# Kernel tuning notes

Measured on AMD Instinct MI355X. Metric: run time of the kernel, lower is better.

Reference implementation:

```python
import jax, jax.numpy as jnp
import numpy as np

B, C, H, W, D = 8, 192, 128, 128, 64


def setup_inputs() -> dict:
    key = jax.random.key(0)
    ks = jax.random.split(key, 9)
    s = 0.1
    return {
        'x': jax.random.normal(ks[0], (B, C, H, W), jnp.float32),
        'Wi': jax.random.normal(ks[1], (D, C), jnp.float32) * s,   # proj_in weight
        'bi': jax.random.normal(ks[2], (D,), jnp.float32) * s,
        'W_ih': jax.random.normal(ks[3], (3 * D, D), jnp.float32) * s,  # GRUCell weight_ih (r,z,n)
        'W_hh': jax.random.normal(ks[4], (3 * D, D), jnp.float32) * s,  # GRUCell weight_hh
        'b_ih': jax.random.normal(ks[5], (3 * D,), jnp.float32) * s,
        'b_hh': jax.random.normal(ks[6], (3 * D,), jnp.float32) * s,
        'Wo': jax.random.normal(ks[7], (C, D), jnp.float32) * s,   # proj_out weight
        'bo': jax.random.normal(ks[8], (C,), jnp.float32) * s,
    }


def _gru_scan(seq, W_ih, W_hh, b_ih, b_hh):
    # seq: (N, T, D). PyTorch GRUCell gate order: r, z, n.
    N, T, Dh = seq.shape[0], seq.shape[1], W_hh.shape[1]
    x_gates = jnp.einsum('ntd,gd->ntg', seq, W_ih) + b_ih  # (N, T, 3D), precomputed
    h0 = jnp.zeros((N, Dh), seq.dtype)

    def step(h, xg):
        hg = h @ W_hh.T + b_hh
        xr, xz, xn = jnp.split(xg, 3, axis=-1)
        hr, hz, hn = jnp.split(hg, 3, axis=-1)
        r = jax.nn.sigmoid(xr + hr)
        z = jax.nn.sigmoid(xz + hz)
        n = jnp.tanh(xn + r * hn)
        h_new = (1.0 - z) * n + z * h
        return h_new, h_new

    _, hs = jax.lax.scan(step, h0, jnp.swapaxes(x_gates, 0, 1))  # (T, N, D)
    return jnp.swapaxes(hs, 0, 1)  # (N, T, D)


def _scan_direction(x, Wi, bi, W_ih, W_hh, b_ih, b_hh, Wo, bo, transpose, reverse):
    b, c, h, w = x.shape
    # arrange to (B, A, T, C): scan along T (W for row scans, H for column scans)
    xs = jnp.transpose(x, (0, 3, 2, 1)) if transpose else jnp.transpose(x, (0, 2, 3, 1))
    if reverse:
        xs = xs[:, :, ::-1, :]
    A, T = xs.shape[1], xs.shape[2]
    seq = xs.reshape(b * A, T, c) @ Wi.T + bi              # proj_in -> (N, T, D)
    hs = _gru_scan(seq, W_ih, W_hh, b_ih, b_hh)            # (N, T, D)
    out = hs @ Wo.T + bo                                   # proj_out -> (N, T, C)
    out = out.reshape(b, A, T, c)
    if reverse:
        out = out[:, :, ::-1, :]
    return jnp.transpose(out, (0, 3, 2, 1)) if transpose else jnp.transpose(out, (0, 3, 1, 2))


def reference(x, Wi, bi, W_ih, W_hh, b_ih, b_hh, Wo, bo):
    p = (Wi, bi, W_ih, W_hh, b_ih, b_hh, Wo, bo)
    right = _scan_direction(x, *p, transpose=False, reverse=False)
    down = _scan_direction(x, *p, transpose=True, reverse=False)
    left = _scan_direction(x, *p, transpose=False, reverse=True)
    up = _scan_direction(x, *p, transpose=True, reverse=True)
    return (right + down + left + up) / 4.0
```

## Files before the change

kernel.cpp:

```cpp
#include <hip/hip_runtime.h>

#define Cn   192
#define Dn   64
#define G3   192
#define HWn  16384
#define NSp  131072L
#define Tn   128

typedef unsigned short u16;
typedef __attribute__((ext_vector_type(8))) short s8v;
typedef __attribute__((ext_vector_type(4))) float f4v;

__device__ __forceinline__ float bf2f(u16 u){
  union { unsigned int i; float f; } v; v.i = ((unsigned int)u) << 16; return v.f;
}
__device__ __forceinline__ u16 f2bf(float f){
  union { float f; unsigned int u; } v; v.f = f;
  return (u16)((v.u + 0x7FFFu + ((v.u >> 16) & 1u)) >> 16);
}
__device__ __forceinline__ s8v load8_f32_as_bf16(const float* __restrict__ p){
  s8v r;
  #pragma unroll
  for (int i = 0; i < 8; i++) r[i] = (short)f2bf(p[i]);
  return r;
}
__device__ __forceinline__ float ex2f(float x){
#if __has_builtin(__builtin_amdgcn_exp2f)
  return __builtin_amdgcn_exp2f(x);
#else
  float r; asm("v_exp_f32 %0, %1" : "=v"(r) : "v"(x)); return r;
#endif
}
__device__ __forceinline__ float rcpa(float x){
#if __has_builtin(__builtin_amdgcn_rcpf)
  return __builtin_amdgcn_rcpf(x);
#else
  float r; asm("v_rcp_f32 %0, %1" : "=v"(r) : "v"(x)); return r;
#endif
}

#define SC_RZ (-1.4426950408889634f)
#define SC_N  (-2.8853900817779268f)

__global__ __launch_bounds__(256) void k_wcomb(const float* __restrict__ Wi, const float* __restrict__ bi,
                                               const float* __restrict__ W_ih, const float* __restrict__ b_ih,
                                               u16* __restrict__ wcomb, float* __restrict__ bcomb){
  if (blockIdx.x < 144) {
    int idx = blockIdx.x * 256 + threadIdx.x;
    int g = idx / 192, c = idx - g * 192;
    float acc = 0.f;
    #pragma unroll 8
    for (int d = 0; d < 64; d++)
      acc += W_ih[g * 64 + d] * Wi[d * 192 + c];
    float sc = (g >= 128) ? SC_N : SC_RZ;
    wcomb[g * 192 + c] = f2bf(sc * acc);
  } else if (threadIdx.x < 192) {
    int g = threadIdx.x;
    float acc = b_ih[g];
    for (int d = 0; d < 64; d++)
      acc += W_ih[g * 64 + d] * bi[d];
    float sc = (g >= 128) ? SC_N : SC_RZ;
    bcomb[g] = sc * acc;
  }
}

__global__ __launch_bounds__(256) void k_gates(const float* __restrict__ x, const u16* __restrict__ wcomb,
                                               const float* __restrict__ bcomb, u16* __restrict__ G){
  __shared__ u16 xT[64][200];
  const int tid = threadIdx.x;
  const int wave = tid >> 6, lane = tid & 63;
  const int col = lane & 15, kq = lane >> 4;
  const long s0 = (long)blockIdx.x * 64;
  const int b   = (int)(s0 >> 14);
  const int hw0 = (int)(s0 & 16383);

  s8v bfrag[3][6];
  #pragma unroll
  for (int j = 0; j < 3; j++) {
    int g = wave * 48 + j * 16 + col;
    #pragma unroll
    for (int kc = 0; kc < 6; kc++)
      bfrag[j][kc] = *(const s8v*)(wcomb + g * 192 + kc * 32 + kq * 8);
  }

  for (int idx = tid; idx < 192 * 16; idx += 256) {
    int c  = idx >> 4;
    int s4 = (idx & 15) * 4;
    float4 v = *(const float4*)(x + (long)(b * 192 + c) * HWn + hw0 + s4);
    xT[s4 + 0][c] = f2bf(v.x); xT[s4 + 1][c] = f2bf(v.y);
    xT[s4 + 2][c] = f2bf(v.z); xT[s4 + 3][c] = f2bf(v.w);
  }
  __syncthreads();

  f4v acc[4][3];
  #pragma unroll
  for (int m = 0; m < 4; m++)
    #pragma unroll
    for (int j = 0; j < 3; j++) acc[m][j] = (f4v){0.f, 0.f, 0.f, 0.f};

  #pragma unroll
  for (int kc = 0; kc < 6; kc++) {
    #pragma unroll
    for (int m = 0; m < 4; m++) {
      s8v a = *(const s8v*)(&xT[m * 16 + col][kc * 32 + kq * 8]);
      #pragma unroll
      for (int j = 0; j < 3; j++)
        acc[m][j] = __builtin_amdgcn_mfma_f32_16x16x32_bf16(a, bfrag[j][kc], acc[m][j], 0, 0, 0);
    }
  }

  #pragma unroll
  for (int j = 0; j < 3; j++) {
    int g = wave * 48 + j * 16 + col;
    float bias = bcomb[g];
    #pragma unroll
    for (int m = 0; m < 4; m++) {
      #pragma unroll
      for (int r = 0; r < 4; r++) {
        long srow = s0 + m * 16 + kq * 4 + r;
        G[srow * 192 + g] = f2bf(acc[m][j][r] + bias);
      }
    }
  }
}

__global__ __launch_bounds__(256) void k_scan(const u16* __restrict__ G, const float* __restrict__ W_hh,
                                              const float* __restrict__ b_hh, u16* __restrict__ Hall){
  __shared__ u16 ha[2][16][72];
  const int tid = threadIdx.x;
  const int w = tid >> 6, lane = tid & 63;
  const int col = lane & 15, kq = lane >> 4;
  const int dir  = blockIdx.x >> 6;
  const int sblk = blockIdx.x & 63;
  const int doff = 16 * w + 4 * kq;

  s8v afrag[3][2];
  f4v biasf[3];
  #pragma unroll
  for (int g3 = 0; g3 < 3; g3++) {
    float sc = (g3 == 2) ? SC_N : SC_RZ;
    const float* wr = W_hh + (g3 * 64 + 16 * w + col) * 64;
    #pragma unroll
    for (int kc = 0; kc < 2; kc++) {
      s8v f;
      #pragma unroll
      for (int i = 0; i < 4; i++) f[i]     = (short)f2bf(sc * wr[kc * 32 +      4 * kq + i]);
      #pragma unroll
      for (int i = 0; i < 4; i++) f[4 + i] = (short)f2bf(sc * wr[kc * 32 + 16 + 4 * kq + i]);
      afrag[g3][kc] = f;
    }
    const float* bb = b_hh + g3 * 64 + doff;
    biasf[g3] = (f4v){ sc * bb[0], sc * bb[1], sc * bb[2], sc * bb[3] };
  }

  const int seq = sblk * 16 + col;
  const int b = seq >> 7, a = seq & 127;
  long base; int stride;
  if ((dir & 1) == 0) { base = ((long)(b * 128 + a)) * 128; stride = 1;   }
  else                { base = (long)b * 16384 + a;         stride = 128; }
  const int rev = dir >> 1;
  u16* __restrict__ Hs = Hall + (long)dir * (NSp * 64);

  for (int i = tid; i < 2 * 16 * 72; i += 256) ((u16*)ha)[i] = 0;
  float hold[4] = {0.f, 0.f, 0.f, 0.f};

  uint2 xr, xz, xn;
  {
    int tp = rev ? 127 : 0;
    const u16* gp = G + (base + (long)tp * stride) * 192 + doff;
    xr = *(const uint2*)(gp);
    xz = *(const uint2*)(gp + 64);
    xn = *(const uint2*)(gp + 128);
  }
  __syncthreads();

  int p = 0;
  for (int t = 0; t < 128; t++) {
    uint2 nxr, nxz, nxn;
    if (t < 127) {
      int tp2 = rev ? (126 - t) : (t + 1);
      const u16* gp2 = G + (base + (long)tp2 * stride) * 192 + doff;
      nxr = *(const uint2*)(gp2);
      nxz = *(const uint2*)(gp2 + 64);
      nxn = *(const uint2*)(gp2 + 128);
    }

    union BU { ushort4 q[2]; s8v v; } u0, u1;
    u0.q[0] = *(const ushort4*)(&ha[p][col][ 0 + 4 * kq]);
    u0.q[1] = *(const ushort4*)(&ha[p][col][16 + 4 * kq]);
    u1.q[0] = *(const ushort4*)(&ha[p][col][32 + 4 * kq]);
    u1.q[1] = *(const ushort4*)(&ha[p][col][48 + 4 * kq]);

    f4v acc0 = biasf[0], acc1 = biasf[1], acc2 = biasf[2];
    acc0 = __builtin_amdgcn_mfma_f32_16x16x32_bf16(afrag[0][0], u0.v, acc0, 0, 0, 0);
    acc1 = __builtin_amdgcn_mfma_f32_16x16x32_bf16(afrag[1][0], u0.v, acc1, 0, 0, 0);
    acc2 = __builtin_amdgcn_mfma_f32_16x16x32_bf16(afrag[2][0], u0.v, acc2, 0, 0, 0);
    acc0 = __builtin_amdgcn_mfma_f32_16x16x32_bf16(afrag[0][1], u1.v, acc0, 0, 0, 0);
    acc1 = __builtin_amdgcn_mfma_f32_16x16x32_bf16(afrag[1][1], u1.v, acc1, 0, 0, 0);
    acc2 = __builtin_amdgcn_mfma_f32_16x16x32_bf16(afrag[2][1], u1.v, acc2, 0, 0, 0);

    u16* px = (u16*)&xr; u16* pz = (u16*)&xz; u16* pn = (u16*)&xn;
    ushort4 hv; u16* hvp = (u16*)&hv;
    #pragma unroll
    for (int r = 0; r < 4; r++) {
      float rr = rcpa(1.f + ex2f(bf2f(px[r]) + acc0[r]));
      float zz = rcpa(1.f + ex2f(bf2f(pz[r]) + acc1[r]));
      float nn = 2.f * rcpa(1.f + ex2f(bf2f(pn[r]) + rr * acc2[r])) - 1.f;
      float h  = nn + zz * (hold[r] - nn);
      hold[r] = h;
      hvp[r] = f2bf(h);
    }

    *(ushort4*)(&ha[p ^ 1][col][doff]) = hv;
    long posc = base + (long)(rev ? (127 - t) : t) * stride;
    *(ushort4*)(Hs + posc * 64 + doff) = hv;
    if (t < 127) { xr = nxr; xz = nxz; xn = nxn; }
    __syncthreads();
    p ^= 1;
  }
}

__global__ __launch_bounds__(256) void k_out(const u16* __restrict__ Hall, const float* __restrict__ Wo,
                                             const float* __restrict__ bo, float* __restrict__ out){
  __shared__ u16 hs4[64][72];
  const int tid = threadIdx.x;
  const int wave = tid >> 6, lane = tid & 63;
  const int col = lane & 15, kq = lane >> 4;
  const long s0 = (long)blockIdx.x * 64;
  const int b   = (int)(s0 >> 14);
  const int hw0 = (int)(s0 & 16383);

  s8v bfrag[3][2]; f4v biasf[3];
  #pragma unroll
  for (int j = 0; j < 3; j++) {
    int g = wave * 48 + j * 16 + col;
    bfrag[j][0] = load8_f32_as_bf16(Wo + g * 64 + kq * 8);
    bfrag[j][1] = load8_f32_as_bf16(Wo + g * 64 + 32 + kq * 8);
    float bb = bo[g];
    biasf[j] = (f4v){bb, bb, bb, bb};
  }

  for (int idx = tid; idx < 64 * 16; idx += 256) {
    int sl = idx >> 4;
    int d4 = (idx & 15) * 4;
    long p = (s0 + sl) * 64 + d4;
    float a0 = 0.f, a1 = 0.f, a2 = 0.f, a3 = 0.f;
    #pragma unroll
    for (int dd = 0; dd < 4; dd++) {
      uint2 v = *(const uint2*)(Hall + dd * (NSp * 64) + p);
      u16* pv = (u16*)&v;
      a0 += bf2f(pv[0]); a1 += bf2f(pv[1]); a2 += bf2f(pv[2]); a3 += bf2f(pv[3]);
    }
    ushort4 o;
    o.x = f2bf(0.25f * a0); o.y = f2bf(0.25f * a1);
    o.z = f2bf(0.25f * a2); o.w = f2bf(0.25f * a3);
    *(ushort4*)(&hs4[sl][d4]) = o;
  }
  __syncthreads();

  f4v acc[4][3];
  #pragma unroll
  for (int m = 0; m < 4; m++)
    #pragma unroll
    for (int j = 0; j < 3; j++) acc[m][j] = biasf[j];

  #pragma unroll
  for (int kc = 0; kc < 2; kc++) {
    #pragma unroll
    for (int m = 0; m < 4; m++) {
      s8v a = *(const s8v*)(&hs4[m * 16 + col][kc * 32 + kq * 8]);
      #pragma unroll
      for (int j = 0; j < 3; j++)
        acc[m][j] = __builtin_amdgcn_mfma_f32_16x16x32_bf16(a, bfrag[j][kc], acc[m][j], 0, 0, 0);
    }
  }

  #pragma unroll
  for (int j = 0; j < 3; j++) {
    int g = wave * 48 + j * 16 + col;
    #pragma unroll
    for (int m = 0; m < 4; m++) {
      float4 v;
      v.x = acc[m][j][0]; v.y = acc[m][j][1];
      v.z = acc[m][j][2]; v.w = acc[m][j][3];
      long addr = ((long)(b * 192 + g) << 14) + hw0 + m * 16 + kq * 4;
      *(float4*)(out + addr) = v;
    }
  }
}

extern "C" void kernel_launch(void* const* d_in, const int* in_sizes, int n_in,
                              void* d_out, int out_size, void* d_ws, size_t ws_size,
                              hipStream_t stream){
  const float* x    = (const float*)d_in[0];
  const float* Wi   = (const float*)d_in[1];
  const float* bi   = (const float*)d_in[2];
  const float* W_ih = (const float*)d_in[3];
  const float* W_hh = (const float*)d_in[4];
  const float* b_ih = (const float*)d_in[5];
  const float* b_hh = (const float*)d_in[6];
  const float* Wo   = (const float*)d_in[7];
  const float* bo   = (const float*)d_in[8];

  char* ws = (char*)d_ws;
  u16*   wcomb = (u16*)(ws);
  float* bcomb = (float*)(ws + 73728);
  u16*   G     = (u16*)(ws + 74496);
  u16*   Hall  = (u16*)(ws + 50406144);

  k_wcomb<<<145,  256, 0, stream>>>(Wi, bi, W_ih, b_ih, wcomb, bcomb);
  k_gates<<<2048, 256, 0, stream>>>(x, wcomb, bcomb, G);
  k_scan <<<256,  256, 0, stream>>>(G, W_hh, b_hh, Hall);
  k_out  <<<2048, 256, 0, stream>>>(Hall, Wo, bo, (float*)d_out);
}
```

Baseline: 332.3 us.

## Run GRU scan in one wave with hidden state kept in MFMA registers

The recurrent scan kernel now uses a single 64-thread wave per block of 16 sequences instead of four waves. Each step's new hidden state is packed to bf16 and fed directly as the MFMA B operand from registers. This drops the shared-memory round trip and the per-step __syncthreads barrier. The r/z hidden biases are folded into the precomputed gate bias. In exchange, each wave issues four times as many MFMAs and gate evaluations per step, which lengthens per-step work on each CU and raises register pressure.

New measurement: 376.5 us. 1.13x slower.

```diff
diff --git a/kernel.cpp b/kernel.cpp
--- a/kernel.cpp
+++ b/kernel.cpp
@@ -44,6 +44,7 @@
 
 __global__ __launch_bounds__(256) void k_wcomb(const float* __restrict__ Wi, const float* __restrict__ bi,
                                                const float* __restrict__ W_ih, const float* __restrict__ b_ih,
+                                               const float* __restrict__ b_hh,
                                                u16* __restrict__ wcomb, float* __restrict__ bcomb){
   if (blockIdx.x < 144) {
     int idx = blockIdx.x * 256 + threadIdx.x;
@@ -59,6 +60,7 @@
     float acc = b_ih[g];
     for (int d = 0; d < 64; d++)
       acc += W_ih[g * 64 + d] * bi[d];
+    if (g < 128) acc += b_hh[g];
     float sc = (g >= 128) ? SC_N : SC_RZ;
     bcomb[g] = sc * acc;
   }
@@ -124,22 +126,18 @@
   }
 }
 
-__global__ __launch_bounds__(256) void k_scan(const u16* __restrict__ G, const float* __restrict__ W_hh,
-                                              const float* __restrict__ b_hh, u16* __restrict__ Hall){
-  __shared__ u16 ha[2][16][72];
-  const int tid = threadIdx.x;
-  const int w = tid >> 6, lane = tid & 63;
+__global__ __launch_bounds__(64, 1) void k_scan(const u16* __restrict__ G, const float* __restrict__ W_hh,
+                                                const float* __restrict__ b_hh, u16* __restrict__ Hall){
+  const int lane = threadIdx.x & 63;
   const int col = lane & 15, kq = lane >> 4;
   const int dir  = blockIdx.x >> 6;
   const int sblk = blockIdx.x & 63;
-  const int doff = 16 * w + 4 * kq;
-
-  s8v afrag[3][2];
-  f4v biasf[3];
-  #pragma unroll
-  for (int g3 = 0; g3 < 3; g3++) {
-    float sc = (g3 == 2) ? SC_N : SC_RZ;
-    const float* wr = W_hh + (g3 * 64 + 16 * w + col) * 64;
+
+  s8v afrag[12][2];
+  #pragma unroll
+  for (int j = 0; j < 12; j++) {
+    float sc = (j >= 8) ? SC_N : SC_RZ;
+    const float* wr = W_hh + (j * 16 + col) * 64;
     #pragma unroll
     for (int kc = 0; kc < 2; kc++) {
       s8v f;
@@ -147,10 +145,14 @@
       for (int i = 0; i < 4; i++) f[i]     = (short)f2bf(sc * wr[kc * 32 +      4 * kq + i]);
       #pragma unroll
       for (int i = 0; i < 4; i++) f[4 + i] = (short)f2bf(sc * wr[kc * 32 + 16 + 4 * kq + i]);
-      afrag[g3][kc] = f;
-    }
-    const float* bb = b_hh + g3 * 64 + doff;
-    biasf[g3] = (f4v){ sc * bb[0], sc * bb[1], sc * bb[2], sc * bb[3] };
+      afrag[j][kc] = f;
+    }
+  }
+  f4v biasn[4];
+  #pragma unroll
+  for (int jp = 0; jp < 4; jp++) {
+    const float* bb = b_hh + 128 + jp * 16 + 4 * kq;
+    biasn[jp] = (f4v){SC_N * bb[0], SC_N * bb[1], SC_N * bb[2], SC_N * bb[3]};
   }
 
   const int seq = sblk * 16 + col;
@@ -159,64 +161,83 @@
   if ((dir & 1) == 0) { base = ((long)(b * 128 + a)) * 128; stride = 1;   }
   else                { base = (long)b * 16384 + a;         stride = 128; }
   const int rev = dir >> 1;
+  const long pd = rev ? -(long)stride : (long)stride;
   u16* __restrict__ Hs = Hall + (long)dir * (NSp * 64);
 
-  for (int i = tid; i < 2 * 16 * 72; i += 256) ((u16*)ha)[i] = 0;
-  float hold[4] = {0.f, 0.f, 0.f, 0.f};
-
-  uint2 xr, xz, xn;
-  {
-    int tp = rev ? 127 : 0;
-    const u16* gp = G + (base + (long)tp * stride) * 192 + doff;
-    xr = *(const uint2*)(gp);
-    xz = *(const uint2*)(gp + 64);
-    xn = *(const uint2*)(gp + 128);
-  }
-  __syncthreads();
-
-  int p = 0;
+  const long pos0 = base + (long)(rev ? 127 : 0) * stride;
+  const u16* gq = G  + pos0 * 192 + 4 * kq;
+  u16*       hq = Hs + pos0 * 64  + 4 * kq;
+
+  uint2 xc[12];
+  #pragma unroll
+  for (int g3 = 0; g3 < 3; g3++)
+    #pragma unroll
+    for (int jp = 0; jp < 4; jp++)
+      xc[g3 * 4 + jp] = *(const uint2*)(gq + g3 * 64 + jp * 16);
+
+  float hold[16];
+  #pragma unroll
+  for (int i = 0; i < 16; i++) hold[i] = 0.f;
+  union BW { unsigned int u[4]; s8v v; } ba, bb2;
+  #pragma unroll
+  for (int i = 0; i < 4; i++) { ba.u[i] = 0u; bb2.u[i] = 0u; }
+
   for (int t = 0; t < 128; t++) {
-    uint2 nxr, nxz, nxn;
+    uint2 nx[12];
     if (t < 127) {
-      int tp2 = rev ? (126 - t) : (t + 1);
-      const u16* gp2 = G + (base + (long)tp2 * stride) * 192 + doff;
-      nxr = *(const uint2*)(gp2);
-      nxz = *(const uint2*)(gp2 + 64);
-      nxn = *(const uint2*)(gp2 + 128);
-    }
-
-    union BU { ushort4 q[2]; s8v v; } u0, u1;
-    u0.q[0] = *(const ushort4*)(&ha[p][col][ 0 + 4 * kq]);
-    u0.q[1] = *(const ushort4*)(&ha[p][col][16 + 4 * kq]);
-    u1.q[0] = *(const ushort4*)(&ha[p][col][32 + 4 * kq]);
-    u1.q[1] = *(const ushort4*)(&ha[p][col][48 + 4 * kq]);
-
-    f4v acc0 = biasf[0], acc1 = biasf[1], acc2 = biasf[2];
-    acc0 = __builtin_amdgcn_mfma_f32_16x16x32_bf16(afrag[0][0], u0.v, acc0, 0, 0, 0);
-    acc1 = __builtin_amdgcn_mfma_f32_16x16x32_bf16(afrag[1][0], u0.v, acc1, 0, 0, 0);
-    acc2 = __builtin_amdgcn_mfma_f32_16x16x32_bf16(afrag[2][0], u0.v, acc2, 0, 0, 0);
-    acc0 = __builtin_amdgcn_mfma_f32_16x16x32_bf16(afrag[0][1], u1.v, acc0, 0, 0, 0);
-    acc1 = __builtin_amdgcn_mfma_f32_16x16x32_bf16(afrag[1][1], u1.v, acc1, 0, 0, 0);
-    acc2 = __builtin_amdgcn_mfma_f32_16x16x32_bf16(afrag[2][1], u1.v, acc2, 0, 0, 0);
-
-    u16* px = (u16*)&xr; u16* pz = (u16*)&xz; u16* pn = (u16*)&xn;
-    ushort4 hv; u16* hvp = (u16*)&hv;
-    #pragma unroll
-    for (int r = 0; r < 4; r++) {
-      float rr = rcpa(1.f + ex2f(bf2f(px[r]) + acc0[r]));
-      float zz = rcpa(1.f + ex2f(bf2f(pz[r]) + acc1[r]));
-      float nn = 2.f * rcpa(1.f + ex2f(bf2f(pn[r]) + rr * acc2[r])) - 1.f;
-      float h  = nn + zz * (hold[r] - nn);
-      hold[r] = h;
-      hvp[r] = f2bf(h);
-    }
-
-    *(ushort4*)(&ha[p ^ 1][col][doff]) = hv;
-    long posc = base + (long)(rev ? (127 - t) : t) * stride;
-    *(ushort4*)(Hs + posc * 64 + doff) = hv;
-    if (t < 127) { xr = nxr; xz = nxz; xn = nxn; }
-    __syncthreads();
-    p ^= 1;
+      gq += pd * 192;
+      #pragma unroll
+      for (int g3 = 0; g3 < 3; g3++)
+        #pragma unroll
+        for (int jp = 0; jp < 4; jp++)
+          nx[g3 * 4 + jp] = *(const uint2*)(gq + g3 * 64 + jp * 16);
+    }
+
+    f4v acc[12];
+    #pragma unroll
+    for (int j = 0; j < 8; j++) acc[j] = (f4v){0.f, 0.f, 0.f, 0.f};
+    #pragma unroll
+    for (int jp = 0; jp < 4; jp++) acc[8 + jp] = biasn[jp];
+    #pragma unroll
+    for (int jp = 0; jp < 4; jp++) {
+      acc[jp]     = __builtin_amdgcn_mfma_f32_16x16x32_bf16(afrag[jp][0],     ba.v,  acc[jp],     0, 0, 0);
+      acc[4 + jp] = __builtin_amdgcn_mfma_f32_16x16x32_bf16(afrag[4 + jp][0], ba.v,  acc[4 + jp], 0, 0, 0);
+      acc[8 + jp] = __builtin_amdgcn_mfma_f32_16x16x32_bf16(afrag[8 + jp][0], ba.v,  acc[8 + jp], 0, 0, 0);
+      acc[jp]     = __builtin_amdgcn_mfma_f32_16x16x32_bf16(afrag[jp][1],     bb2.v, acc[jp],     0, 0, 0);
+      acc[4 + jp] = __builtin_amdgcn_mfma_f32_16x16x32_bf16(afrag[4 + jp][1], bb2.v, acc[4 + jp], 0, 0, 0);
+      acc[8 + jp] = __builtin_amdgcn_mfma_f32_16x16x32_bf16(afrag[8 + jp][1], bb2.v, acc[8 + jp], 0, 0, 0);
+    }
+
+    #pragma unroll
+    for (int jp = 0; jp < 4; jp++) {
+      const u16* pxr = (const u16*)&xc[jp];
+      const u16* pxz = (const u16*)&xc[4 + jp];
+      const u16* pxn = (const u16*)&xc[8 + jp];
+      float hh[4];
+      #pragma unroll
+      for (int r = 0; r < 4; r++) {
+        float rr = rcpa(1.f + ex2f(bf2f(pxr[r]) + acc[jp][r]));
+        float zz = rcpa(1.f + ex2f(bf2f(pxz[r]) + acc[4 + jp][r]));
+        float nn = 2.f * rcpa(1.f + ex2f(bf2f(pxn[r]) + rr * acc[8 + jp][r])) - 1.f;
+        float h  = nn + zz * (hold[jp * 4 + r] - nn);
+        hold[jp * 4 + r] = h;
+        hh[r] = h;
+      }
+      unsigned int w0, w1;
+      asm("v_cvt_pk_bf16_f32 %0, %1, %2" : "=v"(w0) : "v"(hh[0]), "v"(hh[1]));
+      asm("v_cvt_pk_bf16_f32 %0, %1, %2" : "=v"(w1) : "v"(hh[2]), "v"(hh[3]));
+      if (jp == 0)      { ba.u[0]  = w0; ba.u[1]  = w1; }
+      else if (jp == 1) { ba.u[2]  = w0; ba.u[3]  = w1; }
+      else if (jp == 2) { bb2.u[0] = w0; bb2.u[1] = w1; }
+      else              { bb2.u[2] = w0; bb2.u[3] = w1; }
+      uint2 wv; wv.x = w0; wv.y = w1;
+      *(uint2*)(hq + jp * 16) = wv;
+    }
+    hq += pd * 64;
+    if (t < 127) {
+      #pragma unroll
+      for (int i = 0; i < 12; i++) xc[i] = nx[i];
+    }
   }
 }
 
@@ -308,8 +329,8 @@
   u16*   G     = (u16*)(ws + 74496);
   u16*   Hall  = (u16*)(ws + 50406144);
 
-  k_wcomb<<<145,  256, 0, stream>>>(Wi, bi, W_ih, b_ih, wcomb, bcomb);
+  k_wcomb<<<145,  256, 0, stream>>>(Wi, bi, W_ih, b_ih, b_hh, wcomb, bcomb);
   k_gates<<<2048, 256, 0, stream>>>(x, wcomb, bcomb, G);
-  k_scan <<<256,  256, 0, stream>>>(G, W_hh, b_hh, Hall);
+  k_scan <<<256,   64, 0, stream>>>(G, W_hh, b_hh, Hall);
   k_out  <<<2048, 256, 0, stream>>>(Hall, Wo, bo, (float*)d_out);
 }
```

## Deepen gate prefetch, fold r/z hidden bias into gates, trim scan barrier

Applied to the files above, without the earlier changes.

The scan kernel now prefetches gate inputs two timesteps ahead instead of one and walks the gate and output arrays with incremented pointers rather than recomputing addresses each step. The r and z parts of b_hh are folded into the precomputed gate bias so their accumulators start at zero. Hidden-state packing uses v_cvt_pk_bf16_f32, and the loop ends with an explicit lgkmcnt wait, s_barrier and sched_barrier instead of __syncthreads. The goal is to shorten the serial per-step latency of the recurrence, at the cost of a few more live registers. Because the folded bias is now rounded to bf16 together with G, numerics change slightly.

Measured after the change: 306.1 us. 7.9% less time.

```diff
diff --git a/kernel.cpp b/kernel.cpp
--- a/kernel.cpp
+++ b/kernel.cpp
@@ -44,6 +44,7 @@
 
 __global__ __launch_bounds__(256) void k_wcomb(const float* __restrict__ Wi, const float* __restrict__ bi,
                                                const float* __restrict__ W_ih, const float* __restrict__ b_ih,
+                                               const float* __restrict__ b_hh,
                                                u16* __restrict__ wcomb, float* __restrict__ bcomb){
   if (blockIdx.x < 144) {
     int idx = blockIdx.x * 256 + threadIdx.x;
@@ -59,6 +60,7 @@
     float acc = b_ih[g];
     for (int d = 0; d < 64; d++)
       acc += W_ih[g * 64 + d] * bi[d];
+    if (g < 128) acc += b_hh[g];
     float sc = (g >= 128) ? SC_N : SC_RZ;
     bcomb[g] = sc * acc;
   }
@@ -135,7 +137,6 @@
   const int doff = 16 * w + 4 * kq;
 
   s8v afrag[3][2];
-  f4v biasf[3];
   #pragma unroll
   for (int g3 = 0; g3 < 3; g3++) {
     float sc = (g3 == 2) ? SC_N : SC_RZ;
@@ -149,8 +150,11 @@
       for (int i = 0; i < 4; i++) f[4 + i] = (short)f2bf(sc * wr[kc * 32 + 16 + 4 * kq + i]);
       afrag[g3][kc] = f;
     }
-    const float* bb = b_hh + g3 * 64 + doff;
-    biasf[g3] = (f4v){ sc * bb[0], sc * bb[1], sc * bb[2], sc * bb[3] };
+  }
+  f4v biasn;
+  {
+    const float* bb = b_hh + 128 + doff;
+    biasn = (f4v){SC_N * bb[0], SC_N * bb[1], SC_N * bb[2], SC_N * bb[3]};
   }
 
   const int seq = sblk * 16 + col;
@@ -159,39 +163,39 @@
   if ((dir & 1) == 0) { base = ((long)(b * 128 + a)) * 128; stride = 1;   }
   else                { base = (long)b * 16384 + a;         stride = 128; }
   const int rev = dir >> 1;
+  const long pd = rev ? -(long)stride : (long)stride;
   u16* __restrict__ Hs = Hall + (long)dir * (NSp * 64);
+  const long pos0 = base + (long)(rev ? 127 : 0) * stride;
+  const u16* gq = G  + pos0 * 192 + doff;
+  u16*       hq = Hs + pos0 * 64  + doff;
 
   for (int i = tid; i < 2 * 16 * 72; i += 256) ((u16*)ha)[i] = 0;
+
   float hold[4] = {0.f, 0.f, 0.f, 0.f};
 
-  uint2 xr, xz, xn;
-  {
-    int tp = rev ? 127 : 0;
-    const u16* gp = G + (base + (long)tp * stride) * 192 + doff;
-    xr = *(const uint2*)(gp);
-    xz = *(const uint2*)(gp + 64);
-    xn = *(const uint2*)(gp + 128);
-  }
+  uint2 xr0, xz0, xn0, xr1, xz1, xn1;
+  xr0 = *(const uint2*)(gq); xz0 = *(const uint2*)(gq + 64); xn0 = *(const uint2*)(gq + 128);
+  gq += pd * 192;
+  xr1 = *(const uint2*)(gq); xz1 = *(const uint2*)(gq + 64); xn1 = *(const uint2*)(gq + 128);
   __syncthreads();
 
   int p = 0;
   for (int t = 0; t < 128; t++) {
     uint2 nxr, nxz, nxn;
-    if (t < 127) {
-      int tp2 = rev ? (126 - t) : (t + 1);
-      const u16* gp2 = G + (base + (long)tp2 * stride) * 192 + doff;
-      nxr = *(const uint2*)(gp2);
-      nxz = *(const uint2*)(gp2 + 64);
-      nxn = *(const uint2*)(gp2 + 128);
-    }
-
-    union BU { ushort4 q[2]; s8v v; } u0, u1;
+    if (t < 126) {
+      gq += pd * 192;
+      nxr = *(const uint2*)(gq); nxz = *(const uint2*)(gq + 64); nxn = *(const uint2*)(gq + 128);
+    }
+
+    union BW { ushort4 q[2]; s8v v; } u0, u1;
     u0.q[0] = *(const ushort4*)(&ha[p][col][ 0 + 4 * kq]);
     u0.q[1] = *(const ushort4*)(&ha[p][col][16 + 4 * kq]);
     u1.q[0] = *(const ushort4*)(&ha[p][col][32 + 4 * kq]);
     u1.q[1] = *(const ushort4*)(&ha[p][col][48 + 4 * kq]);
 
-    f4v acc0 = biasf[0], acc1 = biasf[1], acc2 = biasf[2];
+    f4v acc0 = (f4v){0.f, 0.f, 0.f, 0.f};
+    f4v acc1 = (f4v){0.f, 0.f, 0.f, 0.f};
+    f4v acc2 = biasn;
     acc0 = __builtin_amdgcn_mfma_f32_16x16x32_bf16(afrag[0][0], u0.v, acc0, 0, 0, 0);
     acc1 = __builtin_amdgcn_mfma_f32_16x16x32_bf16(afrag[1][0], u0.v, acc1, 0, 0, 0);
     acc2 = __builtin_amdgcn_mfma_f32_16x16x32_bf16(afrag[2][0], u0.v, acc2, 0, 0, 0);
@@ -199,23 +203,32 @@
     acc1 = __builtin_amdgcn_mfma_f32_16x16x32_bf16(afrag[1][1], u1.v, acc1, 0, 0, 0);
     acc2 = __builtin_amdgcn_mfma_f32_16x16x32_bf16(afrag[2][1], u1.v, acc2, 0, 0, 0);
 
-    u16* px = (u16*)&xr; u16* pz = (u16*)&xz; u16* pn = (u16*)&xn;
-    ushort4 hv; u16* hvp = (u16*)&hv;
+    const u16* pxr = (const u16*)&xr0;
+    const u16* pxz = (const u16*)&xz0;
+    const u16* pxn = (const u16*)&xn0;
+    float hh[4];
     #pragma unroll
     for (int r = 0; r < 4; r++) {
-      float rr = rcpa(1.f + ex2f(bf2f(px[r]) + acc0[r]));
-      float zz = rcpa(1.f + ex2f(bf2f(pz[r]) + acc1[r]));
-      float nn = 2.f * rcpa(1.f + ex2f(bf2f(pn[r]) + rr * acc2[r])) - 1.f;
+      float rr = rcpa(1.f + ex2f(bf2f(pxr[r]) + acc0[r]));
+      float zz = rcpa(1.f + ex2f(bf2f(pxz[r]) + acc1[r]));
+      float nn = 2.f * rcpa(1.f + ex2f(bf2f(pxn[r]) + rr * acc2[r])) - 1.f;
       float h  = nn + zz * (hold[r] - nn);
-      hold[r] = h;
-      hvp[r] = f2bf(h);
-    }
-
-    *(ushort4*)(&ha[p ^ 1][col][doff]) = hv;
-    long posc = base + (long)(rev ? (127 - t) : t) * stride;
-    *(ushort4*)(Hs + posc * 64 + doff) = hv;
-    if (t < 127) { xr = nxr; xz = nxz; xn = nxn; }
-    __syncthreads();
+      hold[r] = h; hh[r] = h;
+    }
+    unsigned int w0, w1;
+    asm("v_cvt_pk_bf16_f32 %0, %1, %2" : "=v"(w0) : "v"(hh[0]), "v"(hh[1]));
+    asm("v_cvt_pk_bf16_f32 %0, %1, %2" : "=v"(w1) : "v"(hh[2]), "v"(hh[3]));
+    uint2 wv; wv.x = w0; wv.y = w1;
+    *(uint2*)(&ha[p ^ 1][col][doff]) = wv;
+    *(uint2*)(hq) = wv;
+    hq += pd * 64;
+
+    xr0 = xr1; xz0 = xz1; xn0 = xn1;
+    if (t < 126) { xr1 = nxr; xz1 = nxz; xn1 = nxn; }
+
+    asm volatile("s_waitcnt lgkmcnt(0)" ::: "memory");
+    __builtin_amdgcn_s_barrier();
+    __builtin_amdgcn_sched_barrier(0);
     p ^= 1;
   }
 }
@@ -308,7 +321,7 @@
   u16*   G     = (u16*)(ws + 74496);
   u16*   Hall  = (u16*)(ws + 50406144);
 
-  k_wcomb<<<145,  256, 0, stream>>>(Wi, bi, W_ih, b_ih, wcomb, bcomb);
+  k_wcomb<<<145,  256, 0, stream>>>(Wi, bi, W_ih, b_ih, b_hh, wcomb, bcomb);
   k_gates<<<2048, 256, 0, stream>>>(x, wcomb, bcomb, G);
   k_scan <<<256,  256, 0, stream>>>(G, W_hh, b_hh, Hall);
   k_out  <<<2048, 256, 0, stream>>>(Hall, Wo, bo, (float*)d_out);
```
